# Kernel optimization log

Measured on AMD Instinct MI355X. Metric: run time of the kernel, lower is better.

Reference implementation:

```python
import jax, jax.numpy as jnp
import numpy as np

N_POINTS = 262144
SP_FEAT = 128
HIDDEN = 64
EMBED = 256
NUM_SP = 4096
NUM_SP2 = 256
PAD_LIMIT = 64
MASK_RATIO = 0.6


def setup_inputs() -> dict:
    key = jax.random.key(0)
    ks = jax.random.split(key, 6)
    x = jax.random.normal(ks[0], (N_POINTS, SP_FEAT), jnp.float32)
    # point -> superpoint ids, sorted; force every superpoint non-empty
    idx10 = jax.random.randint(ks[1], (N_POINTS,), 0, NUM_SP)
    idx10 = jnp.sort(idx10.at[:NUM_SP].set(jnp.arange(NUM_SP))).astype(jnp.int32)
    # superpoint -> higher superpoint, balanced (16 per group, < PAD_LIMIT), sorted
    idx21 = ((jnp.arange(NUM_SP) * NUM_SP2) // NUM_SP).astype(jnp.int32)
    # deterministic mask: exactly int(NUM_SP * MASK_RATIO) superpoints masked
    mask_num = int(NUM_SP * MASK_RATIO)
    perm = jax.random.permutation(ks[2], NUM_SP)
    is_masked = jnp.zeros((NUM_SP,), bool).at[perm[:mask_num]].set(True)
    W1 = jax.random.normal(ks[3], (SP_FEAT, HIDDEN), jnp.float32) / np.sqrt(SP_FEAT).astype(np.float32)
    b1 = jnp.zeros((HIDDEN,), jnp.float32)
    W2 = jax.random.normal(ks[4], (HIDDEN, EMBED), jnp.float32) / np.sqrt(HIDDEN).astype(np.float32)
    b2 = jnp.zeros((EMBED,), jnp.float32)
    return {
        "full_features": x,
        "full_super_indices_10": idx10,
        "full_super_indices_21": idx21,
        "is_masked": is_masked,
        "W1": W1, "b1": b1, "W2": W2, "b2": b2,
    }


def _pad_scatter(tokens, idx21, flag):
    # tokens: [NUM_SP, C]; idx21 sorted sp->sp2 ids; flag: [NUM_SP] bool.
    # rank of each flagged superpoint within its sp2 group (in sp order)
    f = flag.astype(jnp.int32)
    cum = jnp.cumsum(f)                                            # inclusive global cumsum
    per_group = jax.ops.segment_sum(f, idx21, num_segments=NUM_SP2)
    prefix = jnp.concatenate([jnp.zeros((1,), jnp.int32), jnp.cumsum(per_group)[:-1]])
    rank = cum - 1 - prefix[idx21]                                 # 0-based slot within group
    slot = jnp.where(flag, rank, PAD_LIMIT)                        # PAD_LIMIT -> dropped
    out = jnp.zeros((NUM_SP2, PAD_LIMIT, tokens.shape[-1]), tokens.dtype)
    return out.at[idx21, slot].set(tokens, mode="drop")


def reference(full_features, full_super_indices_10, full_super_indices_21,
              is_masked, W1, b1, W2, b2):
    # per-point 2-layer MLP (gather is implicit: MLP is pointwise), then segment max
    h = jax.nn.relu(full_features @ W1 + b1)                       # [N, HIDDEN]
    h = jax.nn.relu(h @ W2 + b2)                                   # [N, EMBED]
    tok = jax.ops.segment_max(h, full_super_indices_10, num_segments=NUM_SP)  # [NUM_SP, EMBED]
    remain_tokens = _pad_scatter(tok, full_super_indices_21, ~is_masked)      # [NUM_SP2, PAD, EMBED]
    mask_tokens = _pad_scatter(tok, full_super_indices_21, is_masked)         # [NUM_SP2, PAD, EMBED]
    return (remain_tokens, mask_tokens)
```

## Files before the change

kernel.cpp:

```cpp
#include <hip/hip_runtime.h>
#include <hip/hip_bf16.h>

#define N_POINTS 262144
#define SP_FEAT 128
#define HIDDEN 64
#define EMBED 256
#define NUM_SP 4096
#define NUM_SP2 256
#define PAD_LIMIT 64
#define SLOTS 4
#define XS_STRIDE 136
#define H1_STRIDE 76
#define LOCAL_SP 8

typedef __bf16 bf16x8 __attribute__((ext_vector_type(8)));
typedef float floatx4 __attribute__((ext_vector_type(4)));
using bf16 = __hip_bfloat16;

__global__ __launch_bounds__(256) void fused_prep_kernel(
    const float* __restrict__ W1, const float* __restrict__ W2,
    const int* __restrict__ idx10, const int* __restrict__ idx21,
    const void* __restrict__ is_masked,
    bf16* __restrict__ W1t, bf16* __restrict__ W2t,
    int* __restrict__ start, int* __restrict__ invR, int* __restrict__ invM)
{
    const int tid = threadIdx.x;
    const int blk = blockIdx.x;

    if (blk < 256) {
        int p0 = (blk * 256 + tid) * 4;
        int4 v = *(const int4*)(idx10 + p0);
        if (p0 == 0) { start[0] = 0; start[NUM_SP] = N_POINTS; }
        if (v.y != v.x) start[v.y] = p0 + 1;
        if (v.z != v.y) start[v.z] = p0 + 2;
        if (v.w != v.z) start[v.w] = p0 + 3;
        if (p0 + 4 < N_POINTS) {
            int nx = idx10[p0 + 4];
            if (nx != v.w) start[nx] = p0 + 4;
        }
        return;
    }
    if (blk < 352) {
        int i = (blk - 256) * 256 + tid;
        if (i < HIDDEN * SP_FEAT) {
            int n = i >> 7, k = i & 127;
            W1t[i] = __float2bfloat16(W1[k * HIDDEN + n]);
        } else {
            int j = i - HIDDEN * SP_FEAT;
            int n = j >> 6, k = j & 63;
            W2t[j] = __float2bfloat16(W2[k * EMBED + n]);
        }
        return;
    }
    __shared__ int encS;
    if (tid == 0) encS = 0;
    __syncthreads();
    const unsigned char* mb = (const unsigned char*)is_masked;
    const int* mi = (const int*)is_masked;
    int local = 0;
    for (int p = tid; p < NUM_SP; p += 256)
        if ((p & 3) && mb[p]) local = 1;
    if (local) atomicOr(&encS, 1);
    __syncthreads();
    const int e = encS;

    const int g = tid;
    int a = 0, b = NUM_SP;
    while (a < b) { int m = (a + b) >> 1; if (idx21[m] < g) a = m + 1; else b = m; }
    int lo = a;
    b = NUM_SP;
    while (a < b) { int m = (a + b) >> 1; if (idx21[m] < g + 1) a = m + 1; else b = m; }
    int hi = a;
    int nR = 0, nM = 0;
    for (int s = lo; s < hi; ++s) {
        int msk = e ? (int)mb[s] : mi[s];
        if (msk) { if (nM < PAD_LIMIT) invM[g * PAD_LIMIT + nM] = s; nM++; }
        else     { if (nR < PAD_LIMIT) invR[g * PAD_LIMIT + nR] = s; nR++; }
    }
    for (int r = nR; r < PAD_LIMIT; ++r) invR[g * PAD_LIMIT + r] = -1;
    for (int r = nM; r < PAD_LIMIT; ++r) invM[g * PAD_LIMIT + r] = -1;
}

__global__ __launch_bounds__(256, 4) void mlp_segmax_kernel(
    const float* __restrict__ X, const int* __restrict__ idx10,
    const int* __restrict__ start,
    const bf16* __restrict__ W1t, const float* __restrict__ b1,
    const bf16* __restrict__ W2t, const float* __restrict__ b2,
    float* __restrict__ partial)
{
    __shared__ __align__(16) bf16 Xs[64][XS_STRIDE];
    __shared__ __align__(16) bf16 H1s[64][H1_STRIDE];
    __shared__ int tokL[LOCAL_SP][EMBED];
    __shared__ int sIdx[64];

    const int tid  = threadIdx.x;
    const int lane = tid & 63;
    const int w    = tid >> 6;
    const int l15  = lane & 15;
    const int quad = lane >> 4;
    const int b    = blockIdx.x;
    const int m0   = b * 64;

#pragma unroll
    for (int j = 0; j < LOCAL_SP; ++j) tokL[j][tid] = 0;

    bf16x8 bw1[4];
    {
        const bf16* p = W1t + (16 * w + l15) * SP_FEAT + quad * 8;
#pragma unroll
        for (int ks = 0; ks < 4; ++ks) bw1[ks] = *(const bf16x8*)(p + 32 * ks);
    }
    bf16x8 bf2[4][2];
#pragma unroll
    for (int tn = 0; tn < 4; ++tn) {
        const bf16* p = W2t + (64 * w + 16 * tn + l15) * HIDDEN + quad * 8;
#pragma unroll
        for (int ks = 0; ks < 2; ++ks) bf2[tn][ks] = *(const bf16x8*)(p + 32 * ks);
    }
    float b2f[4];
#pragma unroll
    for (int tn = 0; tn < 4; ++tn) b2f[tn] = b2[64 * w + 16 * tn + l15];
    const float b1v = b1[16 * w + l15];

#pragma unroll
    for (int i = 0; i < 4; ++i) {
        int c   = tid + 256 * i;
        int row = c >> 4;
        int cc  = (c & 15) * 8;
        const float* src = X + (size_t)(m0 + row) * SP_FEAT + cc;
        float4 u0 = *(const float4*)src;
        float4 u1 = *(const float4*)(src + 4);
        union { bf16x8 v; bf16 h[8]; } u;
        u.h[0] = __float2bfloat16(u0.x); u.h[1] = __float2bfloat16(u0.y);
        u.h[2] = __float2bfloat16(u0.z); u.h[3] = __float2bfloat16(u0.w);
        u.h[4] = __float2bfloat16(u1.x); u.h[5] = __float2bfloat16(u1.y);
        u.h[6] = __float2bfloat16(u1.z); u.h[7] = __float2bfloat16(u1.w);
        *(bf16x8*)(&Xs[row][cc]) = u.v;
    }
    if (tid < 64) sIdx[tid] = idx10[m0 + tid];
    __syncthreads();

    floatx4 zero4 = {0.f, 0.f, 0.f, 0.f};
    floatx4 acc1[4] = {zero4, zero4, zero4, zero4};
#pragma unroll
    for (int ks = 0; ks < 4; ++ks) {
        int k = ks * 32 + quad * 8;
#pragma unroll
        for (int tm = 0; tm < 4; ++tm) {
            bf16x8 a = *(bf16x8*)(&Xs[16 * tm + l15][k]);
            acc1[tm] = __builtin_amdgcn_mfma_f32_16x16x32_bf16(a, bw1[ks], acc1[tm], 0, 0, 0);
        }
    }
#pragma unroll
    for (int tm = 0; tm < 4; ++tm) {
#pragma unroll
        for (int r = 0; r < 4; ++r) {
            float v = acc1[tm][r] + b1v;
            v = v > 0.f ? v : 0.f;
            H1s[16 * tm + quad * 4 + r][16 * w + l15] = __float2bfloat16(v);
        }
    }
    __syncthreads();

    bf16x8 afr[4][2];
    int sps[16];
#pragma unroll
    for (int tm = 0; tm < 4; ++tm) {
        afr[tm][0] = *(bf16x8*)(&H1s[16 * tm + l15][quad * 8]);
        afr[tm][1] = *(bf16x8*)(&H1s[16 * tm + l15][32 + quad * 8]);
        int4 s4 = *(const int4*)(&sIdx[16 * tm + 4 * quad]);
        sps[4 * tm + 0] = s4.x; sps[4 * tm + 1] = s4.y;
        sps[4 * tm + 2] = s4.z; sps[4 * tm + 3] = s4.w;
    }
    const int sp0 = sIdx[0];

#pragma unroll
    for (int tn = 0; tn < 4; ++tn) {
        const int col = 64 * w + 16 * tn + l15;
        int cur_sp = -1;
        float cur = 0.f;
#pragma unroll
        for (int tm = 0; tm < 4; ++tm) {
            floatx4 acc = zero4;
            acc = __builtin_amdgcn_mfma_f32_16x16x32_bf16(afr[tm][0], bf2[tn][0], acc, 0, 0, 0);
            acc = __builtin_amdgcn_mfma_f32_16x16x32_bf16(afr[tm][1], bf2[tn][1], acc, 0, 0, 0);
#pragma unroll
            for (int r = 0; r < 4; ++r) {
                float v = acc[r] + b2f[tn];
                v = v > 0.f ? v : 0.f;
                int sp = sps[4 * tm + r];
                if (sp == cur_sp) {
                    cur = fmaxf(cur, v);
                } else {
                    if (cur_sp >= 0) {
                        int local = cur_sp - sp0;
                        if (local < LOCAL_SP) {
                            atomicMax(&tokL[local][col], __float_as_int(cur));
                        } else {
                            int slot = b - (start[cur_sp] >> 6);
                            atomicMax((int*)(partial + ((size_t)cur_sp * SLOTS +
                                      (slot < 3 ? slot : 3)) * EMBED + col),
                                      __float_as_int(cur));
                        }
                    }
                    cur_sp = sp;
                    cur = v;
                }
            }
        }
        {
            int local = cur_sp - sp0;
            if (local < LOCAL_SP) {
                atomicMax(&tokL[local][col], __float_as_int(cur));
            } else {
                int slot = b - (start[cur_sp] >> 6);
                atomicMax((int*)(partial + ((size_t)cur_sp * SLOTS +
                          (slot < 3 ? slot : 3)) * EMBED + col),
                          __float_as_int(cur));
            }
        }
    }
    __syncthreads();

    int nsp = sIdx[63] - sp0 + 1;
    if (nsp > LOCAL_SP) nsp = LOCAL_SP;
    for (int j = 0; j < nsp; ++j) {
        int sp   = sp0 + j;
        int slot = b - (start[sp] >> 6);
        int bits = tokL[j][tid];
        int* dst = (int*)(partial + ((size_t)sp * SLOTS + (slot < 3 ? slot : 3)) * EMBED + tid);
        if (slot < 3) *dst = bits;
        else atomicMax(dst, bits);
    }
}

__global__ __launch_bounds__(256) void scatter_kernel(
    const float4* __restrict__ partial4, const int* __restrict__ start,
    const int* __restrict__ invR, const int* __restrict__ invM,
    float4* __restrict__ out4)
{
    const int bb   = blockIdx.x;
    const int g    = bb & (NUM_SP2 - 1);
    const int slab = bb >> 8;
    const int tid  = threadIdx.x;
    const int c4   = tid & 63;
    const int r0   = tid >> 6;
    const int* tab = slab ? invM : invR;
    float4* o = out4 + ((size_t)slab * NUM_SP2 + g) * PAD_LIMIT * 64;
#pragma unroll 4
    for (int rr = 0; rr < 16; ++rr) {
        int row = r0 + rr * 4;
        int sp = tab[g * PAD_LIMIT + row];
        float4 v = {0.f, 0.f, 0.f, 0.f};
        if (sp >= 0) {
            int sb = start[sp] >> 6;
            int se = (start[sp + 1] - 1) >> 6;
            int ns = se - sb;
            const float4* p = partial4 + (size_t)sp * SLOTS * 64 + c4;
            v = p[0];
            if (ns > 0) {
                float4 q = p[64];
                v.x = fmaxf(v.x, q.x); v.y = fmaxf(v.y, q.y);
                v.z = fmaxf(v.z, q.z); v.w = fmaxf(v.w, q.w);
            }
            if (ns > 1) {
                float4 q = p[128];
                v.x = fmaxf(v.x, q.x); v.y = fmaxf(v.y, q.y);
                v.z = fmaxf(v.z, q.z); v.w = fmaxf(v.w, q.w);
            }
            if (ns > 2) {
                float4 q = p[192];
                v.x = fmaxf(v.x, q.x); v.y = fmaxf(v.y, q.y);
                v.z = fmaxf(v.z, q.z); v.w = fmaxf(v.w, q.w);
            }
        }
        o[row * 64 + c4] = v;
    }
}

extern "C" void kernel_launch(void* const* d_in, const int* in_sizes, int n_in,
                              void* d_out, int out_size, void* d_ws, size_t ws_size,
                              hipStream_t stream) {
    (void)in_sizes; (void)n_in; (void)ws_size; (void)out_size;
    const float* X        = (const float*)d_in[0];
    const int* idx10      = (const int*)d_in[1];
    const int* idx21      = (const int*)d_in[2];
    const void* is_masked = (const void*)d_in[3];
    const float* W1       = (const float*)d_in[4];
    const float* b1       = (const float*)d_in[5];
    const float* W2       = (const float*)d_in[6];
    const float* b2       = (const float*)d_in[7];

    char* ws       = (char*)d_ws;
    float* partial = (float*)ws;
    bf16* W1t      = (bf16*)(ws + (size_t)NUM_SP * SLOTS * EMBED * 4);
    bf16* W2t      = W1t + HIDDEN * SP_FEAT;
    int*  start    = (int*)((char*)(W2t + EMBED * HIDDEN));
    int*  invR     = start + (NUM_SP + 2);
    int*  invM     = invR + NUM_SP2 * PAD_LIMIT;

    fused_prep_kernel<<<353, 256, 0, stream>>>(
        W1, W2, idx10, idx21, is_masked, W1t, W2t, start, invR, invM);
    mlp_segmax_kernel<<<N_POINTS / 64, 256, 0, stream>>>(
        X, idx10, start, W1t, b1, W2t, b2, partial);
    scatter_kernel<<<NUM_SP2 * 2, 256, 0, stream>>>(
        (const float4*)partial, start, invR, invM, (float4*)d_out);
}
```

Before: 248.2 us.

## Process four tiles per block with register prefetch and uniform-segment fast path

```diff
diff --git a/kernel.cpp b/kernel.cpp
--- a/kernel.cpp
+++ b/kernel.cpp
@@ -12,6 +12,7 @@
 #define XS_STRIDE 136
 #define H1_STRIDE 76
 #define LOCAL_SP 8
+#define TILES 4
 
 typedef __bf16 bf16x8 __attribute__((ext_vector_type(8)));
 typedef float floatx4 __attribute__((ext_vector_type(4)));
@@ -99,7 +100,6 @@
     const int l15  = lane & 15;
     const int quad = lane >> 4;
     const int b    = blockIdx.x;
-    const int m0   = b * 64;
 
 #pragma unroll
     for (int j = 0; j < LOCAL_SP; ++j) tokL[j][tid] = 0;
@@ -122,115 +122,175 @@
     for (int tn = 0; tn < 4; ++tn) b2f[tn] = b2[64 * w + 16 * tn + l15];
     const float b1v = b1[16 * w + l15];
 
-#pragma unroll
-    for (int i = 0; i < 4; ++i) {
-        int c   = tid + 256 * i;
-        int row = c >> 4;
-        int cc  = (c & 15) * 8;
-        const float* src = X + (size_t)(m0 + row) * SP_FEAT + cc;
-        float4 u0 = *(const float4*)src;
-        float4 u1 = *(const float4*)(src + 4);
-        union { bf16x8 v; bf16 h[8]; } u;
-        u.h[0] = __float2bfloat16(u0.x); u.h[1] = __float2bfloat16(u0.y);
-        u.h[2] = __float2bfloat16(u0.z); u.h[3] = __float2bfloat16(u0.w);
-        u.h[4] = __float2bfloat16(u1.x); u.h[5] = __float2bfloat16(u1.y);
-        u.h[6] = __float2bfloat16(u1.z); u.h[7] = __float2bfloat16(u1.w);
-        *(bf16x8*)(&Xs[row][cc]) = u.v;
-    }
-    if (tid < 64) sIdx[tid] = idx10[m0 + tid];
-    __syncthreads();
-
-    floatx4 zero4 = {0.f, 0.f, 0.f, 0.f};
-    floatx4 acc1[4] = {zero4, zero4, zero4, zero4};
-#pragma unroll
-    for (int ks = 0; ks < 4; ++ks) {
-        int k = ks * 32 + quad * 8;
+    const int srow = tid >> 4;
+    const int scc  = (tid & 15) * 8;
+
+    float4 pf0[4], pf1[4];
+    int pfIdx = 0;
+    {
+        const float* xb = X + (size_t)(b * TILES) * 64 * SP_FEAT;
+#pragma unroll
+        for (int i = 0; i < 4; ++i) {
+            const float* src = xb + (size_t)(srow + 16 * i) * SP_FEAT + scc;
+            pf0[i] = *(const float4*)src;
+            pf1[i] = *(const float4*)(src + 4);
+        }
+        if (tid < 64) pfIdx = idx10[(size_t)(b * TILES) * 64 + tid];
+    }
+
+    for (int t = 0; t < TILES; ++t) {
+        const int g4 = b * TILES + t;
+
+#pragma unroll
+        for (int i = 0; i < 4; ++i) {
+            union { bf16x8 v; bf16 h[8]; } u;
+            u.h[0] = __float2bfloat16(pf0[i].x); u.h[1] = __float2bfloat16(pf0[i].y);
+            u.h[2] = __float2bfloat16(pf0[i].z); u.h[3] = __float2bfloat16(pf0[i].w);
+            u.h[4] = __float2bfloat16(pf1[i].x); u.h[5] = __float2bfloat16(pf1[i].y);
+            u.h[6] = __float2bfloat16(pf1[i].z); u.h[7] = __float2bfloat16(pf1[i].w);
+            *(bf16x8*)(&Xs[srow + 16 * i][scc]) = u.v;
+        }
+        if (tid < 64) sIdx[tid] = pfIdx;
+
+        if (t + 1 < TILES) {
+            const float* xb = X + (size_t)(g4 + 1) * 64 * SP_FEAT;
+#pragma unroll
+            for (int i = 0; i < 4; ++i) {
+                const float* src = xb + (size_t)(srow + 16 * i) * SP_FEAT + scc;
+                pf0[i] = *(const float4*)src;
+                pf1[i] = *(const float4*)(src + 4);
+            }
+            if (tid < 64) pfIdx = idx10[(size_t)(g4 + 1) * 64 + tid];
+        }
+        __syncthreads();
+
+        const int sp0  = sIdx[0];
+        const int nsp0 = sIdx[63] - sp0 + 1;
+        const int jn   = nsp0 < LOCAL_SP ? nsp0 : LOCAL_SP;
+        int gsp[4], uni[4];
 #pragma unroll
         for (int tm = 0; tm < 4; ++tm) {
-            bf16x8 a = *(bf16x8*)(&Xs[16 * tm + l15][k]);
-            acc1[tm] = __builtin_amdgcn_mfma_f32_16x16x32_bf16(a, bw1[ks], acc1[tm], 0, 0, 0);
-        }
-    }
-#pragma unroll
-    for (int tm = 0; tm < 4; ++tm) {
-#pragma unroll
-        for (int r = 0; r < 4; ++r) {
-            float v = acc1[tm][r] + b1v;
-            v = v > 0.f ? v : 0.f;
-            H1s[16 * tm + quad * 4 + r][16 * w + l15] = __float2bfloat16(v);
-        }
-    }
-    __syncthreads();
-
-    bf16x8 afr[4][2];
-    int sps[16];
-#pragma unroll
-    for (int tm = 0; tm < 4; ++tm) {
-        afr[tm][0] = *(bf16x8*)(&H1s[16 * tm + l15][quad * 8]);
-        afr[tm][1] = *(bf16x8*)(&H1s[16 * tm + l15][32 + quad * 8]);
-        int4 s4 = *(const int4*)(&sIdx[16 * tm + 4 * quad]);
-        sps[4 * tm + 0] = s4.x; sps[4 * tm + 1] = s4.y;
-        sps[4 * tm + 2] = s4.z; sps[4 * tm + 3] = s4.w;
-    }
-    const int sp0 = sIdx[0];
-
-#pragma unroll
-    for (int tn = 0; tn < 4; ++tn) {
-        const int col = 64 * w + 16 * tn + l15;
-        int cur_sp = -1;
-        float cur = 0.f;
+            gsp[tm] = sIdx[16 * tm];
+            uni[tm] = (gsp[tm] == sIdx[16 * tm + 15]);
+        }
+
+        floatx4 zero4 = {0.f, 0.f, 0.f, 0.f};
+        floatx4 acc1[4] = {zero4, zero4, zero4, zero4};
+#pragma unroll
+        for (int ks = 0; ks < 4; ++ks) {
+            int k = ks * 32 + quad * 8;
+#pragma unroll
+            for (int tm = 0; tm < 4; ++tm) {
+                bf16x8 a = *(bf16x8*)(&Xs[16 * tm + l15][k]);
+                acc1[tm] = __builtin_amdgcn_mfma_f32_16x16x32_bf16(a, bw1[ks], acc1[tm], 0, 0, 0);
+            }
+        }
 #pragma unroll
         for (int tm = 0; tm < 4; ++tm) {
-            floatx4 acc = zero4;
-            acc = __builtin_amdgcn_mfma_f32_16x16x32_bf16(afr[tm][0], bf2[tn][0], acc, 0, 0, 0);
-            acc = __builtin_amdgcn_mfma_f32_16x16x32_bf16(afr[tm][1], bf2[tn][1], acc, 0, 0, 0);
 #pragma unroll
             for (int r = 0; r < 4; ++r) {
-                float v = acc[r] + b2f[tn];
+                float v = acc1[tm][r] + b1v;
                 v = v > 0.f ? v : 0.f;
-                int sp = sps[4 * tm + r];
-                if (sp == cur_sp) {
-                    cur = fmaxf(cur, v);
+                H1s[16 * tm + quad * 4 + r][16 * w + l15] = __float2bfloat16(v);
+            }
+        }
+        __syncthreads();
+
+#pragma unroll
+        for (int tn = 0; tn < 4; ++tn) {
+            const int col = 64 * w + 16 * tn + l15;
+            int cur_sp = -1;
+            float cur = 0.f;
+
+#define FLUSH_G() do { if (cur_sp >= 0) {                                      \
+                float _v = cur + b2f[tn]; _v = _v > 0.f ? _v : 0.f;            \
+                int _loc = cur_sp - sp0;                                       \
+                if (_loc < LOCAL_SP) {                                         \
+                    if (quad == 0) atomicMax(&tokL[_loc][col], __float_as_int(_v)); \
+                } else if (quad == 0) {                                        \
+                    int _sl = g4 - (start[cur_sp] >> 6);                       \
+                    atomicMax((int*)(partial + ((size_t)cur_sp * SLOTS +       \
+                              (_sl < 3 ? _sl : 3)) * EMBED + col),             \
+                              __float_as_int(_v));                             \
+                } } } while (0)
+
+#pragma unroll
+            for (int tm = 0; tm < 4; ++tm) {
+                bf16x8 a0 = *(bf16x8*)(&H1s[16 * tm + l15][quad * 8]);
+                bf16x8 a1 = *(bf16x8*)(&H1s[16 * tm + l15][32 + quad * 8]);
+                floatx4 acc = zero4;
+                acc = __builtin_amdgcn_mfma_f32_16x16x32_bf16(a0, bf2[tn][0], acc, 0, 0, 0);
+                acc = __builtin_amdgcn_mfma_f32_16x16x32_bf16(a1, bf2[tn][1], acc, 0, 0, 0);
+
+                if (uni[tm]) {
+                    float m = fmaxf(fmaxf(acc[0], acc[1]), fmaxf(acc[2], acc[3]));
+                    m = fmaxf(m, __shfl_xor(m, 16, 64));
+                    m = fmaxf(m, __shfl_xor(m, 32, 64));
+                    if (gsp[tm] == cur_sp) {
+                        cur = fmaxf(cur, m);
+                    } else {
+                        FLUSH_G();
+                        cur_sp = gsp[tm];
+                        cur = m;
+                    }
                 } else {
-                    if (cur_sp >= 0) {
-                        int local = cur_sp - sp0;
-                        if (local < LOCAL_SP) {
-                            atomicMax(&tokL[local][col], __float_as_int(cur));
+                    FLUSH_G();
+                    cur_sp = -1;
+                    int lsp = -1;
+                    float lv = 0.f;
+#pragma unroll
+                    for (int r = 0; r < 4; ++r) {
+                        int sp = sIdx[16 * tm + 4 * quad + r];
+                        float v = acc[r];
+                        if (sp == lsp) {
+                            lv = fmaxf(lv, v);
                         } else {
-                            int slot = b - (start[cur_sp] >> 6);
-                            atomicMax((int*)(partial + ((size_t)cur_sp * SLOTS +
-                                      (slot < 3 ? slot : 3)) * EMBED + col),
-                                      __float_as_int(cur));
+                            if (lsp >= 0) {
+                                float _v = lv + b2f[tn]; _v = _v > 0.f ? _v : 0.f;
+                                int _loc = lsp - sp0;
+                                if (_loc < LOCAL_SP) {
+                                    atomicMax(&tokL[_loc][col], __float_as_int(_v));
+                                } else {
+                                    int _sl = g4 - (start[lsp] >> 6);
+                                    atomicMax((int*)(partial + ((size_t)lsp * SLOTS +
+                                              (_sl < 3 ? _sl : 3)) * EMBED + col),
+                                              __float_as_int(_v));
+                                }
+                            }
+                            lsp = sp;
+                            lv = v;
                         }
                     }
-                    cur_sp = sp;
-                    cur = v;
+                    {
+                        float _v = lv + b2f[tn]; _v = _v > 0.f ? _v : 0.f;
+                        int _loc = lsp - sp0;
+                        if (_loc < LOCAL_SP) {
+                            atomicMax(&tokL[_loc][col], __float_as_int(_v));
+                        } else {
+                            int _sl = g4 - (start[lsp] >> 6);
+                            atomicMax((int*)(partial + ((size_t)lsp * SLOTS +
+                                      (_sl < 3 ? _sl : 3)) * EMBED + col),
+                                      __float_as_int(_v));
+                        }
+                    }
                 }
             }
-        }
-        {
-            int local = cur_sp - sp0;
-            if (local < LOCAL_SP) {
-                atomicMax(&tokL[local][col], __float_as_int(cur));
-            } else {
-                int slot = b - (start[cur_sp] >> 6);
-                atomicMax((int*)(partial + ((size_t)cur_sp * SLOTS +
-                          (slot < 3 ? slot : 3)) * EMBED + col),
-                          __float_as_int(cur));
-            }
-        }
-    }
-    __syncthreads();
-
-    int nsp = sIdx[63] - sp0 + 1;
-    if (nsp > LOCAL_SP) nsp = LOCAL_SP;
-    for (int j = 0; j < nsp; ++j) {
-        int sp   = sp0 + j;
-        int slot = b - (start[sp] >> 6);
-        int bits = tokL[j][tid];
-        int* dst = (int*)(partial + ((size_t)sp * SLOTS + (slot < 3 ? slot : 3)) * EMBED + tid);
-        if (slot < 3) *dst = bits;
-        else atomicMax(dst, bits);
+            FLUSH_G();
+#undef FLUSH_G
+        }
+
+        __builtin_amdgcn_wave_barrier();
+
+        for (int j = 0; j < jn; ++j) {
+            int sp   = sp0 + j;
+            int slot = g4 - (start[sp] >> 6);
+            int bits = tokL[j][tid];
+            int* dst = (int*)(partial + ((size_t)sp * SLOTS + (slot < 3 ? slot : 3)) * EMBED + tid);
+            if (slot < 3) *dst = bits;
+            else atomicMax(dst, bits);
+        }
+        if (t + 1 < TILES)
+            for (int j = 0; j < jn; ++j) tokL[j][tid] = 0;
     }
 }
 
@@ -301,7 +361,7 @@
 
     fused_prep_kernel<<<353, 256, 0, stream>>>(
         W1, W2, idx10, idx21, is_masked, W1t, W2t, start, invR, invM);
-    mlp_segmax_kernel<<<N_POINTS / 64, 256, 0, stream>>>(
+    mlp_segmax_kernel<<<N_POINTS / (64 * TILES), 256, 0, stream>>>(
         X, idx10, start, W1t, b1, W2t, b2, partial);
     scatter_kernel<<<NUM_SP2 * 2, 256, 0, stream>>>(
         (const float4*)partial, start, invR, invM, (float4*)d_out);
```

After: 282.9 us. 14.0% more time.
